# Kernel optimization log

Measured on AMD Instinct MI355X. Metric: run time of the kernel, lower is better.

## Reference

```python
import jax, jax.numpy as jnp
import numpy as np

N_NODES = 10000  # static number of graph nodes (segment count)


def setup_inputs() -> dict:
    key = jax.random.key(0)
    ks = jax.random.split(key, 7)
    B, N, DIN, DOUT, E = 2, N_NODES, 256, 256, 320000
    x = jax.random.normal(ks[0], (B, N, DIN), dtype=jnp.float32)
    W = jax.random.normal(ks[1], (DIN, DOUT), dtype=jnp.float32) * (1.0 / np.sqrt(DIN))
    loop_W = jax.random.normal(ks[2], (DIN, DOUT), dtype=jnp.float32) * (1.0 / np.sqrt(DIN))
    bias = jax.random.normal(ks[3], (DOUT,), dtype=jnp.float32) * 0.01
    edge_vals = jax.random.uniform(ks[4], (E,), dtype=jnp.float32)
    rows = jax.random.randint(ks[5], (E,), 0, N, dtype=jnp.int32)
    cols = jax.random.randint(ks[6], (E,), 0, N, dtype=jnp.int32)
    return {"x": x, "W": W, "loop_W": loop_W, "bias": bias,
            "edge_vals": edge_vals, "rows": rows, "cols": cols}


def reference(x, W, loop_W, bias, edge_vals, rows, cols):
    # Dense feature transforms: [b,n,din] @ [din,dout] -> [b,n,dout]
    support = jnp.einsum('bni,io->bno', x, W)
    support_loop = jnp.einsum('bni,io->bno', x, loop_W)
    # Sparse adjacency matmul (COO SpMM): out[r] += val_e * support[:, c_e, :]
    msgs = support[:, cols, :] * edge_vals[None, :, None]      # [b, E, dout]
    agg = jax.ops.segment_sum(
        jnp.swapaxes(msgs, 0, 1), rows, num_segments=N_NODES)   # [n, b, dout]
    agg = jnp.swapaxes(agg, 0, 1)                                # [b, n, dout]
    out = agg + support_loop + bias
    return jax.nn.relu(out)
```

## Files before the change

### kernel.cpp

```cpp
#include <hip/hip_runtime.h>
#include <hip/hip_bf16.h>


#define NN 10000
#define DK 256
#define DO 256
#define MT 20000
#define SCAN_T 1024
#define SCAN_C 10

typedef short short8 __attribute__((ext_vector_type(8)));
typedef float f32x4 __attribute__((ext_vector_type(4)));

__device__ inline unsigned short f2bf(float f) {
    unsigned int u = __float_as_uint(f);
    u = (u + 0x7FFFu + ((u >> 16) & 1u)) >> 16;
    return (unsigned short)u;
}
__device__ inline float bf2f(unsigned short s) {
    return __uint_as_float(((unsigned int)s) << 16);
}

__global__ __launch_bounds__(256) void transpose_w(
    const float* __restrict__ W, const float* __restrict__ LW,
    unsigned short* __restrict__ Wt, unsigned short* __restrict__ LWt,
    int* __restrict__ counts)
{
    __shared__ float tile[64][65];
    const float* src = blockIdx.z ? LW : W;
    unsigned short* dst = blockIdx.z ? LWt : Wt;
    const int k0 = blockIdx.x * 64, c0 = blockIdx.y * 64;

    if (blockIdx.z == 0) {
        const int bid = blockIdx.x * 4 + blockIdx.y;
        const int i = bid * 256 * 3 + threadIdx.x;
        #pragma unroll
        for (int q = 0; q < 3; ++q) {
            const int idx = i + q * 256;
            if (idx < NN) counts[idx] = 0;
        }
    }

    #pragma unroll
    for (int it = 0; it < 16; ++it) {
        const int u = it * 256 + threadIdx.x;
        const int i = u >> 6, j = u & 63;
        tile[i][j] = src[(size_t)(k0 + i) * DO + c0 + j];
    }
    __syncthreads();
    #pragma unroll
    for (int it = 0; it < 16; ++it) {
        const int u = it * 256 + threadIdx.x;
        const int j = u >> 6, i = u & 63;
        dst[(size_t)(c0 + j) * DK + k0 + i] = f2bf(tile[i][j]);
    }
}

__global__ __launch_bounds__(256) void gemm_fused(
    const float* __restrict__ X, const unsigned short* __restrict__ Wt,
    const unsigned short* __restrict__ LWt, const float* __restrict__ bias,
    unsigned short* __restrict__ sup, float* __restrict__ outv)
{
    __shared__ unsigned short As[8][64][8];
    __shared__ unsigned short BsW[8][64][8];
    __shared__ unsigned short BsL[8][64][8];
    const int t = threadIdx.x;
    const int wid = t >> 6, lane = t & 63;
    const int wm = wid >> 1, wn = wid & 1;
    const int m0 = blockIdx.x * 64;
    const int n0 = blockIdx.y * 64;

    f32x4 accW[2][2], accL[2][2];
    #pragma unroll
    for (int i = 0; i < 2; ++i)
        #pragma unroll
        for (int j = 0; j < 2; ++j) {
            accW[i][j] = (f32x4){0.f, 0.f, 0.f, 0.f};
            accL[i][j] = (f32x4){0.f, 0.f, 0.f, 0.f};
        }

    for (int k0 = 0; k0 < DK; k0 += 64) {
        #pragma unroll
        for (int it = 0; it < 2; ++it) {
            const int u = it * 256 + t;
            const int row = u >> 3, kg = u & 7;
            const int grow = m0 + row;
            short8 v = (short8){0,0,0,0,0,0,0,0};
            if (grow < MT) {
                const float4 a = *(const float4*)&X[(size_t)grow * DK + k0 + kg * 8];
                const float4 b = *(const float4*)&X[(size_t)grow * DK + k0 + kg * 8 + 4];
                v[0] = (short)f2bf(a.x); v[1] = (short)f2bf(a.y);
                v[2] = (short)f2bf(a.z); v[3] = (short)f2bf(a.w);
                v[4] = (short)f2bf(b.x); v[5] = (short)f2bf(b.y);
                v[6] = (short)f2bf(b.z); v[7] = (short)f2bf(b.w);
            }
            *(short8*)&As[kg][row ^ kg][0] = v;
        }
        #pragma unroll
        for (int it = 0; it < 2; ++it) {
            const int u = it * 256 + t;
            const int col = u >> 3, kg = u & 7;
            const size_t off = (size_t)(n0 + col) * DK + k0 + kg * 8;
            *(short8*)&BsW[kg][col ^ kg][0] = *(const short8*)&Wt[off];
            *(short8*)&BsL[kg][col ^ kg][0] = *(const short8*)&LWt[off];
        }
        __syncthreads();
        #pragma unroll
        for (int s = 0; s < 2; ++s) {
            const int kg = s * 4 + (lane >> 4);
            short8 af[2], bW[2], bL[2];
            #pragma unroll
            for (int i = 0; i < 2; ++i) {
                const int row = wm * 32 + i * 16 + (lane & 15);
                af[i] = *(const short8*)&As[kg][row ^ kg][0];
            }
            #pragma unroll
            for (int j = 0; j < 2; ++j) {
                const int col = wn * 32 + j * 16 + (lane & 15);
                bW[j] = *(const short8*)&BsW[kg][col ^ kg][0];
                bL[j] = *(const short8*)&BsL[kg][col ^ kg][0];
            }
            #pragma unroll
            for (int i = 0; i < 2; ++i)
                #pragma unroll
                for (int j = 0; j < 2; ++j) {
                    accW[i][j] = __builtin_amdgcn_mfma_f32_16x16x32_bf16(
                        af[i], bW[j], accW[i][j], 0, 0, 0);
                    accL[i][j] = __builtin_amdgcn_mfma_f32_16x16x32_bf16(
                        af[i], bL[j], accL[i][j], 0, 0, 0);
                }
        }
        __syncthreads();
    }

    const int rbase = m0 + wm * 32;
    const int cbase = n0 + wn * 32;
    #pragma unroll
    for (int i = 0; i < 2; ++i)
        #pragma unroll
        for (int q = 0; q < 4; ++q) {
            const int row = rbase + i * 16 + (lane >> 4) * 4 + q;
            if (row < MT) {
                #pragma unroll
                for (int j = 0; j < 2; ++j) {
                    const int col = cbase + j * 16 + (lane & 15);
                    sup[(size_t)row * DO + col] = f2bf(accW[i][j][q]);
                    outv[(size_t)row * DO + col] = accL[i][j][q] + bias[col];
                }
            }
        }
}

__global__ __launch_bounds__(256) void hist_rows(
    const int* __restrict__ rows, int* __restrict__ counts, int E)
{
    const int e = blockIdx.x * 256 + threadIdx.x;
    if (e < E) atomicAdd(&counts[rows[e]], 1);
}

__global__ __launch_bounds__(SCAN_T) void scan_rows(
    const int* __restrict__ counts, int* __restrict__ offsets,
    int* __restrict__ cursor)
{
    __shared__ int sums[SCAN_T];
    const int t = threadIdx.x;
    int local[SCAN_C];
    int s = 0;
    const int base = t * SCAN_C;
    #pragma unroll
    for (int i = 0; i < SCAN_C; ++i) {
        const int idx = base + i;
        const int c = (idx < NN) ? counts[idx] : 0;
        local[i] = s;
        s += c;
    }
    sums[t] = s;
    __syncthreads();
    for (int off = 1; off < SCAN_T; off <<= 1) {
        int u = (t >= off) ? sums[t - off] : 0;
        __syncthreads();
        sums[t] += u;
        __syncthreads();
    }
    const int excl = (t == 0) ? 0 : sums[t - 1];
    #pragma unroll
    for (int i = 0; i < SCAN_C; ++i) {
        const int idx = base + i;
        if (idx < NN) {
            const int o = excl + local[i];
            offsets[idx] = o;
            cursor[idx]  = o;
        }
    }
}

__global__ __launch_bounds__(256) void scatter_edges(
    const int* __restrict__ rows, const int* __restrict__ cols,
    const float* __restrict__ vals, int* __restrict__ cursor,
    float2* __restrict__ epack, int E)
{
    const int e = blockIdx.x * 256 + threadIdx.x;
    if (e >= E) return;
    const int p = atomicAdd(&cursor[rows[e]], 1);
    epack[p] = make_float2(__int_as_float(cols[e]), vals[e]);
}

__global__ __launch_bounds__(256) void agg_relu(
    const unsigned short* __restrict__ sup, const float2* __restrict__ epack,
    const int* __restrict__ offsets, const int* __restrict__ counts,
    float* __restrict__ outv)
{
    const int widx = (blockIdx.x * 256 + threadIdx.x) >> 6;
    if (widx >= 2 * NN) return;
    const int lane = threadIdx.x & 63;
    const int b = widx & 1, r = widx >> 1;
    const int d = lane * 4;
    const size_t supb = (size_t)b * NN * DO + d;
    const int start = offsets[r];
    const int deg   = counts[r];

    float a0 = 0.f, a1 = 0.f, a2 = 0.f, a3 = 0.f;
    #pragma unroll 8
    for (int i = 0; i < deg; ++i) {
        const float2 ep = epack[start + i];
        const int col = __float_as_int(ep.x);
        const float v = ep.y;
        const ushort4 s = *(const ushort4*)&sup[supb + (size_t)col * DO];
        a0 += v * bf2f(s.x); a1 += v * bf2f(s.y);
        a2 += v * bf2f(s.z); a3 += v * bf2f(s.w);
    }

    float* o = &outv[((size_t)b * NN + r) * DO + d];
    float4 t4 = *(const float4*)o;
    t4.x = fmaxf(t4.x + a0, 0.f); t4.y = fmaxf(t4.y + a1, 0.f);
    t4.z = fmaxf(t4.z + a2, 0.f); t4.w = fmaxf(t4.w + a3, 0.f);
    *(float4*)o = t4;
}

extern "C" void kernel_launch(void* const* d_in, const int* in_sizes, int n_in,
                              void* d_out, int out_size, void* d_ws, size_t ws_size,
                              hipStream_t stream)
{
    const float* x    = (const float*)d_in[0];
    const float* W    = (const float*)d_in[1];
    const float* LW   = (const float*)d_in[2];
    const float* bias = (const float*)d_in[3];
    const float* ev   = (const float*)d_in[4];
    const int*   rows = (const int*)d_in[5];
    const int*   cols = (const int*)d_in[6];
    float* out = (float*)d_out;

    const int E = in_sizes[4];

    char* wsb = (char*)d_ws;
    unsigned short* Wt    = (unsigned short*)wsb;
    unsigned short* LWt   = (unsigned short*)(wsb + 131072);
    unsigned short* supb  = (unsigned short*)(wsb + 262144);
    int* counts  = (int*)(wsb + 10502144);
    int* offsets = (int*)(wsb + 10542144);
    int* cursor  = (int*)(wsb + 10582144);
    float2* epack = (float2*)(wsb + 10622144);

    transpose_w<<<dim3(4, 4, 2), 256, 0, stream>>>(W, LW, Wt, LWt, counts);
    hist_rows<<<(E + 255) / 256, 256, 0, stream>>>(rows, counts, E);
    scan_rows<<<1, SCAN_T, 0, stream>>>(counts, offsets, cursor);

    gemm_fused<<<dim3((MT + 63) / 64, DO / 64), 256, 0, stream>>>(
        x, Wt, LWt, bias, supb, out);

    scatter_edges<<<(E + 255) / 256, 256, 0, stream>>>(rows, cols, ev, cursor, epack, E);

    const int aggBlocks = (2 * NN * 64 + 255) / 256;
    agg_relu<<<aggBlocks, 256, 0, stream>>>(supb, epack, offsets, counts, out);
}
```

Before: 128.1 us.

## Merge transpose with histogram and GEMM with edge scatter into combined launches

Merges the weight transpose and the row histogram into one kernel that splits work by block index. It also folds the edge scatter into the GEMM kernel as extra blocks, so independent work shares one launch and can overlap on the GPU. Zeroing of counts moves to a hipMemsetAsync, because the histogram now runs in the same launch. This removes launch gaps and idle tails between small kernels, at the cost of an added memset call and divergent block roles within each kernel.

```diff
diff --git a/kernel.cpp b/kernel.cpp
--- a/kernel.cpp
+++ b/kernel.cpp
@@ -21,54 +21,99 @@
     return __uint_as_float(((unsigned int)s) << 16);
 }
 
-__global__ __launch_bounds__(256) void transpose_w(
+__global__ __launch_bounds__(256) void prep_kernel(
     const float* __restrict__ W, const float* __restrict__ LW,
     unsigned short* __restrict__ Wt, unsigned short* __restrict__ LWt,
-    int* __restrict__ counts)
+    const int* __restrict__ rows, int* __restrict__ counts, int E)
 {
     __shared__ float tile[64][65];
-    const float* src = blockIdx.z ? LW : W;
-    unsigned short* dst = blockIdx.z ? LWt : Wt;
-    const int k0 = blockIdx.x * 64, c0 = blockIdx.y * 64;
-
-    if (blockIdx.z == 0) {
-        const int bid = blockIdx.x * 4 + blockIdx.y;
-        const int i = bid * 256 * 3 + threadIdx.x;
-        #pragma unroll
-        for (int q = 0; q < 3; ++q) {
-            const int idx = i + q * 256;
-            if (idx < NN) counts[idx] = 0;
-        }
-    }
-
-    #pragma unroll
-    for (int it = 0; it < 16; ++it) {
-        const int u = it * 256 + threadIdx.x;
-        const int i = u >> 6, j = u & 63;
-        tile[i][j] = src[(size_t)(k0 + i) * DO + c0 + j];
-    }
+    const int bid = blockIdx.x;
+    if (bid < 32) {
+        const int z = bid >> 4, rem = bid & 15;
+        const int k0 = (rem >> 2) * 64, c0 = (rem & 3) * 64;
+        const float* src = z ? LW : W;
+        unsigned short* dst = z ? LWt : Wt;
+        #pragma unroll
+        for (int it = 0; it < 16; ++it) {
+            const int u = it * 256 + threadIdx.x;
+            const int i = u >> 6, j = u & 63;
+            tile[i][j] = src[(size_t)(k0 + i) * DO + c0 + j];
+        }
+        __syncthreads();
+        #pragma unroll
+        for (int it = 0; it < 16; ++it) {
+            const int u = it * 256 + threadIdx.x;
+            const int j = u >> 6, i = u & 63;
+            dst[(size_t)(c0 + j) * DK + k0 + i] = f2bf(tile[i][j]);
+        }
+    } else {
+        const int e = (bid - 32) * 256 + threadIdx.x;
+        if (e < E) atomicAdd(&counts[rows[e]], 1);
+    }
+}
+
+__global__ __launch_bounds__(SCAN_T) void scan_rows(
+    const int* __restrict__ counts, int* __restrict__ offsets,
+    int* __restrict__ cursor)
+{
+    __shared__ int sums[SCAN_T];
+    const int t = threadIdx.x;
+    int local[SCAN_C];
+    int s = 0;
+    const int base = t * SCAN_C;
+    #pragma unroll
+    for (int i = 0; i < SCAN_C; ++i) {
+        const int idx = base + i;
+        const int c = (idx < NN) ? counts[idx] : 0;
+        local[i] = s;
+        s += c;
+    }
+    sums[t] = s;
     __syncthreads();
-    #pragma unroll
-    for (int it = 0; it < 16; ++it) {
-        const int u = it * 256 + threadIdx.x;
-        const int j = u >> 6, i = u & 63;
-        dst[(size_t)(c0 + j) * DK + k0 + i] = f2bf(tile[i][j]);
-    }
-}
-
-__global__ __launch_bounds__(256) void gemm_fused(
+    for (int off = 1; off < SCAN_T; off <<= 1) {
+        int u = (t >= off) ? sums[t - off] : 0;
+        __syncthreads();
+        sums[t] += u;
+        __syncthreads();
+    }
+    const int excl = (t == 0) ? 0 : sums[t - 1];
+    #pragma unroll
+    for (int i = 0; i < SCAN_C; ++i) {
+        const int idx = base + i;
+        if (idx < NN) {
+            const int o = excl + local[i];
+            offsets[idx] = o;
+            cursor[idx]  = o;
+        }
+    }
+}
+
+__global__ __launch_bounds__(256) void main_kernel(
     const float* __restrict__ X, const unsigned short* __restrict__ Wt,
     const unsigned short* __restrict__ LWt, const float* __restrict__ bias,
-    unsigned short* __restrict__ sup, float* __restrict__ outv)
+    unsigned short* __restrict__ sup, float* __restrict__ outv,
+    const int* __restrict__ rows, const int* __restrict__ cols,
+    const float* __restrict__ vals, int* __restrict__ cursor,
+    float2* __restrict__ epack, int E, int gemmBlocks)
 {
     __shared__ unsigned short As[8][64][8];
     __shared__ unsigned short BsW[8][64][8];
     __shared__ unsigned short BsL[8][64][8];
+
+    if (blockIdx.x >= gemmBlocks) {
+        const int e = (blockIdx.x - gemmBlocks) * 256 + threadIdx.x;
+        if (e < E) {
+            const int p = atomicAdd(&cursor[rows[e]], 1);
+            epack[p] = make_float2(__int_as_float(cols[e]), vals[e]);
+        }
+        return;
+    }
+
     const int t = threadIdx.x;
     const int wid = t >> 6, lane = t & 63;
     const int wm = wid >> 1, wn = wid & 1;
-    const int m0 = blockIdx.x * 64;
-    const int n0 = blockIdx.y * 64;
+    const int m0 = (blockIdx.x >> 2) * 64;
+    const int n0 = (blockIdx.x & 3) * 64;
 
     f32x4 accW[2][2], accL[2][2];
     #pragma unroll
@@ -151,60 +196,6 @@
         }
 }
 
-__global__ __launch_bounds__(256) void hist_rows(
-    const int* __restrict__ rows, int* __restrict__ counts, int E)
-{
-    const int e = blockIdx.x * 256 + threadIdx.x;
-    if (e < E) atomicAdd(&counts[rows[e]], 1);
-}
-
-__global__ __launch_bounds__(SCAN_T) void scan_rows(
-    const int* __restrict__ counts, int* __restrict__ offsets,
-    int* __restrict__ cursor)
-{
-    __shared__ int sums[SCAN_T];
-    const int t = threadIdx.x;
-    int local[SCAN_C];
-    int s = 0;
-    const int base = t * SCAN_C;
-    #pragma unroll
-    for (int i = 0; i < SCAN_C; ++i) {
-        const int idx = base + i;
-        const int c = (idx < NN) ? counts[idx] : 0;
-        local[i] = s;
-        s += c;
-    }
-    sums[t] = s;
-    __syncthreads();
-    for (int off = 1; off < SCAN_T; off <<= 1) {
-        int u = (t >= off) ? sums[t - off] : 0;
-        __syncthreads();
-        sums[t] += u;
-        __syncthreads();
-    }
-    const int excl = (t == 0) ? 0 : sums[t - 1];
-    #pragma unroll
-    for (int i = 0; i < SCAN_C; ++i) {
-        const int idx = base + i;
-        if (idx < NN) {
-            const int o = excl + local[i];
-            offsets[idx] = o;
-            cursor[idx]  = o;
-        }
-    }
-}
-
-__global__ __launch_bounds__(256) void scatter_edges(
-    const int* __restrict__ rows, const int* __restrict__ cols,
-    const float* __restrict__ vals, int* __restrict__ cursor,
-    float2* __restrict__ epack, int E)
-{
-    const int e = blockIdx.x * 256 + threadIdx.x;
-    if (e >= E) return;
-    const int p = atomicAdd(&cursor[rows[e]], 1);
-    epack[p] = make_float2(__int_as_float(cols[e]), vals[e]);
-}
-
 __global__ __launch_bounds__(256) void agg_relu(
     const unsigned short* __restrict__ sup, const float2* __restrict__ epack,
     const int* __restrict__ offsets, const int* __restrict__ counts,
@@ -251,6 +242,8 @@
     float* out = (float*)d_out;
 
     const int E = in_sizes[4];
+    const int EB = (E + 255) / 256;
+    const int gemmBlocks = ((MT + 63) / 64) * 4;
 
     char* wsb = (char*)d_ws;
     unsigned short* Wt    = (unsigned short*)wsb;
@@ -261,14 +254,12 @@
     int* cursor  = (int*)(wsb + 10582144);
     float2* epack = (float2*)(wsb + 10622144);
 
-    transpose_w<<<dim3(4, 4, 2), 256, 0, stream>>>(W, LW, Wt, LWt, counts);
-    hist_rows<<<(E + 255) / 256, 256, 0, stream>>>(rows, counts, E);
+    hipMemsetAsync(counts, 0, NN * sizeof(int), stream);
+
+    prep_kernel<<<32 + EB, 256, 0, stream>>>(W, LW, Wt, LWt, rows, counts, E);
     scan_rows<<<1, SCAN_T, 0, stream>>>(counts, offsets, cursor);
-
-    gemm_fused<<<dim3((MT + 63) / 64, DO / 64), 256, 0, stream>>>(
-        x, Wt, LWt, bias, supb, out);
-
-    scatter_edges<<<(E + 255) / 256, 256, 0, stream>>>(rows, cols, ev, cursor, epack, E);
+    main_kernel<<<gemmBlocks + EB, 256, 0, stream>>>(
+        x, Wt, LWt, bias, supb, out, rows, cols, ev, cursor, epack, E, gemmBlocks);
 
     const int aggBlocks = (2 * NN * 64 + 255) / 256;
     agg_relu<<<aggBlocks, 256, 0, stream>>>(supb, epack, offsets, counts, out);
```

Result: faster. 121.1 us (-5.4%).
